# Optimization experiments

Measured on AMD Instinct MI355X. Metric: run time of the kernel, lower is better.

Reference implementation:

```python
import jax, jax.numpy as jnp
import numpy as np

N_NODES = 50000
N_EDGES = 1600000
IN_FEAT = 128
HEADS = 8
OUT_FEAT = 16


def setup_inputs() -> dict:
    key = jax.random.key(0)
    ks = jax.random.split(key, 8)
    feat = jax.random.normal(ks[0], (N_NODES, IN_FEAT), dtype=jnp.float32)
    src = jax.random.randint(ks[1], (N_EDGES,), 0, N_NODES, dtype=jnp.int32)
    dst = jax.random.randint(ks[2], (N_EDGES,), 0, N_NODES, dtype=jnp.int32)
    eps = jax.random.normal(ks[3], (N_EDGES, HEADS), dtype=jnp.float32)
    # small init scale keeps exp(log_scale) numerically tame
    W_fc = jax.random.normal(ks[4], (IN_FEAT, HEADS * OUT_FEAT), dtype=jnp.float32) * 0.05
    W_post = jax.random.normal(ks[5], (OUT_FEAT, 4), dtype=jnp.float32) * 0.05
    b_post = jax.random.normal(ks[6], (4,), dtype=jnp.float32) * 0.05
    bias = jax.random.normal(ks[7], (HEADS, OUT_FEAT), dtype=jnp.float32) * 0.05
    return {"feat": feat, "src": src, "dst": dst, "eps": eps,
            "W_fc": W_fc, "W_post": W_post, "b_post": b_post, "bias": bias}


def reference(feat, src, dst, eps, W_fc, W_post, b_post, bias):
    N = feat.shape[0]
    # node projection: [N, H, F]
    h = (feat @ W_fc).reshape(N, HEADS, OUT_FEAT)
    # per-node posterior params: [N, H, 4] -> loc_l, loc_r, log_scale_l, log_scale_r
    post = jnp.einsum('nhf,fk->nhk', h, W_post) + b_post
    loc_l, loc_r, lsl, lsr = post[..., 0], post[..., 1], post[..., 2], post[..., 3]
    # per-edge score via reparameterized sample: [E, H]
    loc = loc_l[src] + loc_r[dst]
    log_scale = lsl[src] + lsr[dst]
    e = loc + jnp.exp(log_scale) * eps
    # edge softmax over incoming edges of each dst node (per head)
    m = jax.lax.stop_gradient(jax.ops.segment_max(e, dst, num_segments=N))
    ex = jnp.exp(e - m[dst])
    denom = jax.ops.segment_sum(ex, dst, num_segments=N)
    a = ex / denom[dst]
    # weighted aggregation: sum over in-edges of h[src] * a
    msg = h[src] * a[:, :, None]                     # [E, H, F]
    out = jax.ops.segment_sum(msg, dst, num_segments=N)  # [N, H, F]
    out = out + bias[None]
    return out
```

## Files before the change

### kernel.cpp

```cpp
#include <hip/hip_runtime.h>
#include <hip/hip_fp16.h>

#define IN_FEAT 128
#define HEADS 8
#define OUT_FEAT 16
#define HF 128
#define BSHIFT 6
#define BNODES 64
#define NBMAX 1024
#define CHUNK 8192

__global__ __launch_bounds__(256) void gemm_post_kernel(
    const float* __restrict__ feat, const float* __restrict__ W_fc,
    const float* __restrict__ W_post, const float* __restrict__ b_post,
    __half* __restrict__ hbuf, float* __restrict__ post, int N)
{
    __shared__ float4 lds4[32 * 32];
    float* lds = (float*)lds4;
    const int tid = threadIdx.x;
    const int node_base = blockIdx.x * 32;

    const float4* f4 = (const float4*)feat;
    for (int i = tid; i < 32 * 32; i += 256) {
        int n = i >> 5, k4 = i & 31;
        int gn = node_base + n;
        float4 v = make_float4(0.f, 0.f, 0.f, 0.f);
        if (gn < N) v = f4[gn * 32 + k4];
        lds4[i] = v;
    }
    __syncthreads();

    const int cg = tid & 31, ng = tid >> 5;
    const int n0 = ng * 4;
    float acc[4][4];
#pragma unroll
    for (int i = 0; i < 4; i++) acc[i][0] = acc[i][1] = acc[i][2] = acc[i][3] = 0.f;

    const float4* W4 = (const float4*)W_fc;
#pragma unroll 4
    for (int k = 0; k < 128; ++k) {
        float4 w = W4[k * 32 + cg];
#pragma unroll
        for (int i = 0; i < 4; i++) {
            float f = lds[(n0 + i) * 128 + k];
            acc[i][0] += f * w.x; acc[i][1] += f * w.y;
            acc[i][2] += f * w.z; acc[i][3] += f * w.w;
        }
    }
    __half2* hb2 = (__half2*)hbuf;
#pragma unroll
    for (int i = 0; i < 4; i++) {
        int gn = node_base + n0 + i;
        if (gn < N) {
            union { uint2 u; __half2 h[2]; } pk;
            pk.h[0] = __floats2half2_rn(acc[i][0], acc[i][1]);
            pk.h[1] = __floats2half2_rn(acc[i][2], acc[i][3]);
            *(uint2*)&hb2[gn * 64 + cg * 2] = pk.u;
        }
    }
    __syncthreads();
#pragma unroll
    for (int i = 0; i < 4; i++)
        lds4[(n0 + i) * 32 + cg] = make_float4(acc[i][0], acc[i][1], acc[i][2], acc[i][3]);
    __syncthreads();

    {
        int n = tid >> 3, h = tid & 7;
        float p0 = b_post[0], p1 = b_post[1], p2 = b_post[2], p3 = b_post[3];
#pragma unroll
        for (int f = 0; f < 16; ++f) {
            float v = lds[n * 128 + h * 16 + f];
            p0 += v * W_post[f * 4 + 0];
            p1 += v * W_post[f * 4 + 1];
            p2 += v * W_post[f * 4 + 2];
            p3 += v * W_post[f * 4 + 3];
        }
        int gn = node_base + n;
        if (gn < N) {
            post[gn * 32 + 0 * 8 + h] = p0;
            post[gn * 32 + 1 * 8 + h] = p1;
            post[gn * 32 + 2 * 8 + h] = p2;
            post[gn * 32 + 3 * 8 + h] = p3;
        }
    }
}

__global__ __launch_bounds__(256) void bucket_hist_kernel(
    const int* __restrict__ dst, int* __restrict__ bucket_tot, int E, int nb)
{
    __shared__ int cnt[NBMAX];
    const int tid = threadIdx.x;
    for (int i = tid; i < nb; i += 256) cnt[i] = 0;
    __syncthreads();
    const int stride = gridDim.x * 256;
    for (int g = blockIdx.x * 256 + tid; g < E; g += stride)
        atomicAdd(&cnt[dst[g] >> BSHIFT], 1);
    __syncthreads();
    for (int i = tid; i < nb; i += 256) {
        int c = cnt[i];
        if (c) atomicAdd(&bucket_tot[i], c);
    }
}

__global__ __launch_bounds__(256) void bucket_scan_kernel(
    const int* __restrict__ bucket_tot, int* __restrict__ bucket_base,
    int* __restrict__ bucket_cursor, int nb, int E)
{
    __shared__ int sd[256];
    const int tid = threadIdx.x;
    int v[4]; int s = 0;
#pragma unroll
    for (int k = 0; k < 4; ++k) {
        int i = tid * 4 + k;
        v[k] = (i < nb) ? bucket_tot[i] : 0;
        s += v[k];
    }
    sd[tid] = s;
    __syncthreads();
    for (int off = 1; off < 256; off <<= 1) {
        int t = (tid >= off) ? sd[tid - off] : 0;
        __syncthreads();
        sd[tid] += t;
        __syncthreads();
    }
    int excl = sd[tid] - s;
#pragma unroll
    for (int k = 0; k < 4; ++k) {
        int i = tid * 4 + k;
        if (i < nb) { bucket_base[i] = excl; bucket_cursor[i] = excl; }
        excl += v[k];
    }
    if (tid == 0) bucket_base[nb] = E;
}

__global__ __launch_bounds__(256) void bucket_scatter_kernel(
    const int* __restrict__ src, const int* __restrict__ dst,
    int* __restrict__ bucket_cursor, uint2* __restrict__ recs, int E, int nb)
{
    __shared__ int cnt[NBMAX];
    __shared__ int base[NBMAX];
    const int tid = threadIdx.x;
    for (int i = tid; i < nb; i += 256) cnt[i] = 0;
    __syncthreads();
    const int e0 = blockIdx.x * CHUNK;
    const int e1 = min(e0 + CHUNK, E);
    for (int e = e0 + tid; e < e1; e += 256)
        atomicAdd(&cnt[dst[e] >> BSHIFT], 1);
    __syncthreads();
    for (int i = tid; i < nb; i += 256) {
        int c = cnt[i];
        base[i] = c ? atomicAdd(&bucket_cursor[i], c) : 0;
        cnt[i] = 0;
    }
    __syncthreads();
    for (int e = e0 + tid; e < e1; e += 256) {
        int d = dst[e];
        int b = d >> BSHIFT;
        int slot = base[b] + atomicAdd(&cnt[b], 1);
        recs[slot] = make_uint2((unsigned)e,
                                ((unsigned)src[e] << BSHIFT) | (unsigned)(d & (BNODES - 1)));
    }
}

__global__ __launch_bounds__(256) void bucket_csr_kernel(
    const uint2* __restrict__ recs, const int* __restrict__ bucket_base,
    int* __restrict__ offsets, uint2* __restrict__ csr, int N, int E)
{
    __shared__ int ncnt[BNODES];
    __shared__ int snc[BNODES];
    const int b = blockIdx.x, tid = threadIdx.x;
    const int node_lo = b << BSHIFT;
    const int rlo = bucket_base[b], rhi = bucket_base[b + 1];
    const int gn = node_lo + tid;

    if (tid < BNODES) ncnt[tid] = 0;
    __syncthreads();
    for (int r = rlo + tid; r < rhi; r += 256)
        atomicAdd(&ncnt[recs[r].y & (BNODES - 1u)], 1);
    __syncthreads();
    if (tid < BNODES) snc[tid] = ncnt[tid];
    __syncthreads();
    for (int off = 1; off < BNODES; off <<= 1) {
        int t = (tid < BNODES && tid >= off) ? snc[tid - off] : 0;
        __syncthreads();
        if (tid < BNODES) snc[tid] += t;
        __syncthreads();
    }
    int excl = (tid < BNODES) ? snc[tid] - ncnt[tid] : 0;
    if (tid < BNODES && gn < N) offsets[gn] = rlo + excl;
    if (b == 0 && tid == 0) offsets[N] = E;
    __syncthreads();
    if (tid < BNODES) ncnt[tid] = excl;
    __syncthreads();

    for (int r = rlo + tid; r < rhi; r += 256) {
        uint2 rec = recs[r];
        int dl = (int)(rec.y & (BNODES - 1u));
        unsigned s = rec.y >> BSHIFT;
        int slot = rlo + atomicAdd(&ncnt[dl], 1);
        csr[slot] = make_uint2(rec.x, s);
    }
}

__global__ __launch_bounds__(128) void agg_kernel(
    const uint2* __restrict__ csr, const int* __restrict__ offsets,
    const float* __restrict__ post, const float* __restrict__ eps,
    const __half* __restrict__ hbuf, const float* __restrict__ bias,
    float* __restrict__ out)
{
    __shared__ int    s_src[32];
    __shared__ float  s_a[32 * 9];
    __shared__ float  dpost[16];
    __shared__ float2 r_acc[64];
    __shared__ float  r_dsum[64];

    const int d = blockIdx.x;
    const int tid = threadIdx.x;
    const int wave = tid >> 6, lane = tid & 63;
    const int h = lane >> 3, fp = lane & 7;
    const int start = offsets[d];
    const int deg = offsets[d + 1] - start;

    if (tid < 16)
        dpost[tid] = post[d * 32 + ((tid < 8) ? (8 + tid) : (16 + tid))];
    __syncthreads();

    float2 acc = make_float2(0.f, 0.f);
    float dsum = 0.f;

    const float2* p2 = (const float2*)post;
    const float2* e2 = (const float2*)eps;

    for (int c = 0; c < deg; c += 32) {
        int jc = min(32, deg - c);
        if (tid < 4 * jc) {
            int j = tid >> 2, q = tid & 3;
            uint2 rec = csr[start + c + j];
            int e = (int)rec.x, s = (int)rec.y;
            if (q == 0) s_src[j] = s;
            float2 ll = p2[(size_t)s * 16 + q];
            float2 sl = p2[(size_t)s * 16 + 8 + q];
            float2 ep = e2[(size_t)e * 4 + q];
            int h0 = 2 * q;
            float ev0 = (ll.x + dpost[h0])     + __expf(sl.x + dpost[8 + h0])     * ep.x;
            float ev1 = (ll.y + dpost[h0 + 1]) + __expf(sl.y + dpost[8 + h0 + 1]) * ep.y;
            s_a[j * 9 + h0]     = __expf(ev0);
            s_a[j * 9 + h0 + 1] = __expf(ev1);
        }
        __syncthreads();
        for (int j = wave; j < jc; j += 2) {
            float a = s_a[j * 9 + h];
            const __half2* hr = (const __half2*)(hbuf + (size_t)s_src[j] * 128);
            float2 hv = __half22float2(hr[h * 8 + fp]);
            acc.x += a * hv.x;
            acc.y += a * hv.y;
            dsum  += a;
        }
        __syncthreads();
    }

    if (wave == 0) { r_acc[lane] = acc; r_dsum[lane] = dsum; }
    __syncthreads();
    if (wave == 1) {
        r_acc[lane].x += acc.x;
        r_acc[lane].y += acc.y;
        r_dsum[lane]  += dsum;
    }
    __syncthreads();
    if (wave == 0) {
        float2 A = r_acc[lane];
        float ds = r_dsum[lane];
        float inv = (ds > 0.f) ? 1.f / ds : 0.f;
        float2 o;
        o.x = A.x * inv + bias[h * 16 + 2 * fp];
        o.y = A.y * inv + bias[h * 16 + 2 * fp + 1];
        ((float2*)out)[(size_t)d * 64 + lane] = o;
    }
}

extern "C" void kernel_launch(void* const* d_in, const int* in_sizes, int n_in,
                              void* d_out, int out_size, void* d_ws, size_t ws_size,
                              hipStream_t stream)
{
    const float* feat   = (const float*)d_in[0];
    const int*   src    = (const int*)d_in[1];
    const int*   dst    = (const int*)d_in[2];
    const float* eps    = (const float*)d_in[3];
    const float* W_fc   = (const float*)d_in[4];
    const float* W_post = (const float*)d_in[5];
    const float* b_post = (const float*)d_in[6];
    const float* bias   = (const float*)d_in[7];
    float* out = (float*)d_out;

    const int N = in_sizes[0] / IN_FEAT;
    const int E = in_sizes[1];
    const int nb = (N + BNODES - 1) >> BSHIFT;

    char* p = (char*)d_ws;
    auto alloc = [&](size_t bytes) {
        char* r = p;
        p += (bytes + 255) & ~size_t(255);
        return r;
    };
    __half* hbuf    = (__half*)alloc((size_t)N * HF * 2);
    float*  post    = (float*)alloc((size_t)N * 32 * 4);
    int*    offsets = (int*)alloc((size_t)(N + 1) * 4);
    int*    bucket_tot    = (int*)alloc((size_t)(NBMAX + 1) * 4);
    int*    bucket_base   = (int*)alloc((size_t)(NBMAX + 1) * 4);
    int*    bucket_cursor = (int*)alloc((size_t)(NBMAX + 1) * 4);
    uint2*  recs    = (uint2*)alloc((size_t)E * 8);
    uint2*  csr     = (uint2*)alloc((size_t)E * 8);

    hipMemsetAsync(bucket_tot, 0, (size_t)(nb) * 4, stream);

    gemm_post_kernel<<<(N + 31) / 32, 256, 0, stream>>>(feat, W_fc, W_post, b_post,
                                                        hbuf, post, N);
    bucket_hist_kernel<<<512, 256, 0, stream>>>(dst, bucket_tot, E, nb);
    bucket_scan_kernel<<<1, 256, 0, stream>>>(bucket_tot, bucket_base,
                                              bucket_cursor, nb, E);
    bucket_scatter_kernel<<<(E + CHUNK - 1) / CHUNK, 256, 0, stream>>>(
        src, dst, bucket_cursor, recs, E, nb);
    bucket_csr_kernel<<<nb, 256, 0, stream>>>(recs, bucket_base, offsets, csr, N, E);
    agg_kernel<<<N, 128, 0, stream>>>(csr, offsets, post, eps, hbuf, bias, out);
}
```

Baseline: 360.8 us.

## Build CSR via per-node atomic counts and use one wave per destination node

Replaces the two-pass bucketed scatter (records, then per-bucket CSR) with a per-node histogram, a per-bucket wave scan, and a direct global-atomic scatter into CSR. This drops the intermediate record array and one full pass over the edges. The aggregation kernel is restructured so that one 64-lane wave handles each destination node. Edge scores are computed 8 edges at a time and broadcast with shuffles, which removes the LDS staging and the block-level syncs. The cost is heavy global atomic traffic on cursor[d], and edge order within each node becomes nondeterministic.

```diff
diff --git a/kernel.cpp b/kernel.cpp
--- a/kernel.cpp
+++ b/kernel.cpp
@@ -8,7 +8,6 @@
 #define BSHIFT 6
 #define BNODES 64
 #define NBMAX 1024
-#define CHUNK 8192
 
 __global__ __launch_bounds__(256) void gemm_post_kernel(
     const float* __restrict__ feat, const float* __restrict__ W_fc,
@@ -85,16 +84,20 @@
     }
 }
 
-__global__ __launch_bounds__(256) void bucket_hist_kernel(
-    const int* __restrict__ dst, int* __restrict__ bucket_tot, int E, int nb)
+__global__ __launch_bounds__(256) void hist_kernel(
+    const int* __restrict__ dst, int* __restrict__ ncnt,
+    int* __restrict__ bucket_tot, int E, int nb)
 {
     __shared__ int cnt[NBMAX];
     const int tid = threadIdx.x;
     for (int i = tid; i < nb; i += 256) cnt[i] = 0;
     __syncthreads();
     const int stride = gridDim.x * 256;
-    for (int g = blockIdx.x * 256 + tid; g < E; g += stride)
-        atomicAdd(&cnt[dst[g] >> BSHIFT], 1);
+    for (int g = blockIdx.x * 256 + tid; g < E; g += stride) {
+        int d = dst[g];
+        atomicAdd(&ncnt[d], 1);
+        atomicAdd(&cnt[d >> BSHIFT], 1);
+    }
     __syncthreads();
     for (int i = tid; i < nb; i += 256) {
         int c = cnt[i];
@@ -104,7 +107,7 @@
 
 __global__ __launch_bounds__(256) void bucket_scan_kernel(
     const int* __restrict__ bucket_tot, int* __restrict__ bucket_base,
-    int* __restrict__ bucket_cursor, int nb, int E)
+    int nb, int E)
 {
     __shared__ int sd[256];
     const int tid = threadIdx.x;
@@ -127,155 +130,103 @@
 #pragma unroll
     for (int k = 0; k < 4; ++k) {
         int i = tid * 4 + k;
-        if (i < nb) { bucket_base[i] = excl; bucket_cursor[i] = excl; }
+        if (i < nb) bucket_base[i] = excl;
         excl += v[k];
     }
     if (tid == 0) bucket_base[nb] = E;
 }
 
-__global__ __launch_bounds__(256) void bucket_scatter_kernel(
+__global__ __launch_bounds__(256) void node_scan_kernel(
+    const int* __restrict__ ncnt, const int* __restrict__ bucket_base,
+    int* __restrict__ offsets, int* __restrict__ cursor, int N, int nb, int E)
+{
+    if (blockIdx.x == 0 && threadIdx.x == 0) offsets[N] = E;
+    const int b = blockIdx.x * 4 + (threadIdx.x >> 6);
+    const int lane = threadIdx.x & 63;
+    if (b >= nb) return;
+    const int node = (b << BSHIFT) + lane;
+    int v = (node < N) ? ncnt[node] : 0;
+    int s = v;
+#pragma unroll
+    for (int off = 1; off < 64; off <<= 1) {
+        int t = __shfl_up(s, off, 64);
+        if (lane >= off) s += t;
+    }
+    int excl = bucket_base[b] + s - v;
+    if (node < N) { offsets[node] = excl; cursor[node] = excl; }
+}
+
+__global__ __launch_bounds__(256) void scatter_kernel(
     const int* __restrict__ src, const int* __restrict__ dst,
-    int* __restrict__ bucket_cursor, uint2* __restrict__ recs, int E, int nb)
-{
-    __shared__ int cnt[NBMAX];
-    __shared__ int base[NBMAX];
-    const int tid = threadIdx.x;
-    for (int i = tid; i < nb; i += 256) cnt[i] = 0;
-    __syncthreads();
-    const int e0 = blockIdx.x * CHUNK;
-    const int e1 = min(e0 + CHUNK, E);
-    for (int e = e0 + tid; e < e1; e += 256)
-        atomicAdd(&cnt[dst[e] >> BSHIFT], 1);
-    __syncthreads();
-    for (int i = tid; i < nb; i += 256) {
-        int c = cnt[i];
-        base[i] = c ? atomicAdd(&bucket_cursor[i], c) : 0;
-        cnt[i] = 0;
-    }
-    __syncthreads();
-    for (int e = e0 + tid; e < e1; e += 256) {
+    int* __restrict__ cursor, uint2* __restrict__ csr, int E)
+{
+    const int stride = gridDim.x * 256;
+    for (int e = blockIdx.x * 256 + threadIdx.x; e < E; e += stride) {
         int d = dst[e];
-        int b = d >> BSHIFT;
-        int slot = base[b] + atomicAdd(&cnt[b], 1);
-        recs[slot] = make_uint2((unsigned)e,
-                                ((unsigned)src[e] << BSHIFT) | (unsigned)(d & (BNODES - 1)));
-    }
-}
-
-__global__ __launch_bounds__(256) void bucket_csr_kernel(
-    const uint2* __restrict__ recs, const int* __restrict__ bucket_base,
-    int* __restrict__ offsets, uint2* __restrict__ csr, int N, int E)
-{
-    __shared__ int ncnt[BNODES];
-    __shared__ int snc[BNODES];
-    const int b = blockIdx.x, tid = threadIdx.x;
-    const int node_lo = b << BSHIFT;
-    const int rlo = bucket_base[b], rhi = bucket_base[b + 1];
-    const int gn = node_lo + tid;
-
-    if (tid < BNODES) ncnt[tid] = 0;
-    __syncthreads();
-    for (int r = rlo + tid; r < rhi; r += 256)
-        atomicAdd(&ncnt[recs[r].y & (BNODES - 1u)], 1);
-    __syncthreads();
-    if (tid < BNODES) snc[tid] = ncnt[tid];
-    __syncthreads();
-    for (int off = 1; off < BNODES; off <<= 1) {
-        int t = (tid < BNODES && tid >= off) ? snc[tid - off] : 0;
-        __syncthreads();
-        if (tid < BNODES) snc[tid] += t;
-        __syncthreads();
-    }
-    int excl = (tid < BNODES) ? snc[tid] - ncnt[tid] : 0;
-    if (tid < BNODES && gn < N) offsets[gn] = rlo + excl;
-    if (b == 0 && tid == 0) offsets[N] = E;
-    __syncthreads();
-    if (tid < BNODES) ncnt[tid] = excl;
-    __syncthreads();
-
-    for (int r = rlo + tid; r < rhi; r += 256) {
-        uint2 rec = recs[r];
-        int dl = (int)(rec.y & (BNODES - 1u));
-        unsigned s = rec.y >> BSHIFT;
-        int slot = rlo + atomicAdd(&ncnt[dl], 1);
-        csr[slot] = make_uint2(rec.x, s);
-    }
-}
-
-__global__ __launch_bounds__(128) void agg_kernel(
+        int slot = atomicAdd(&cursor[d], 1);
+        csr[slot] = make_uint2((unsigned)e, (unsigned)src[e]);
+    }
+}
+
+__global__ __launch_bounds__(256) void agg_kernel(
     const uint2* __restrict__ csr, const int* __restrict__ offsets,
     const float* __restrict__ post, const float* __restrict__ eps,
     const __half* __restrict__ hbuf, const float* __restrict__ bias,
-    float* __restrict__ out)
-{
-    __shared__ int    s_src[32];
-    __shared__ float  s_a[32 * 9];
-    __shared__ float  dpost[16];
-    __shared__ float2 r_acc[64];
-    __shared__ float  r_dsum[64];
-
-    const int d = blockIdx.x;
-    const int tid = threadIdx.x;
-    const int wave = tid >> 6, lane = tid & 63;
-    const int h = lane >> 3, fp = lane & 7;
+    float* __restrict__ out, int N)
+{
+    const int lane = threadIdx.x & 63;
+    const int d = blockIdx.x * 4 + (threadIdx.x >> 6);
+    if (d >= N) return;
     const int start = offsets[d];
     const int deg = offsets[d + 1] - start;
-
-    if (tid < 16)
-        dpost[tid] = post[d * 32 + ((tid < 8) ? (8 + tid) : (16 + tid))];
-    __syncthreads();
+    const int j = lane >> 3, hh = lane & 7;
+    const int h = j;
+    const float dl  = post[d * 32 + 8 + hh];
+    const float dls = post[d * 32 + 24 + hh];
 
     float2 acc = make_float2(0.f, 0.f);
     float dsum = 0.f;
 
-    const float2* p2 = (const float2*)post;
-    const float2* e2 = (const float2*)eps;
-
-    for (int c = 0; c < deg; c += 32) {
-        int jc = min(32, deg - c);
-        if (tid < 4 * jc) {
-            int j = tid >> 2, q = tid & 3;
-            uint2 rec = csr[start + c + j];
-            int e = (int)rec.x, s = (int)rec.y;
-            if (q == 0) s_src[j] = s;
-            float2 ll = p2[(size_t)s * 16 + q];
-            float2 sl = p2[(size_t)s * 16 + 8 + q];
-            float2 ep = e2[(size_t)e * 4 + q];
-            int h0 = 2 * q;
-            float ev0 = (ll.x + dpost[h0])     + __expf(sl.x + dpost[8 + h0])     * ep.x;
-            float ev1 = (ll.y + dpost[h0 + 1]) + __expf(sl.y + dpost[8 + h0 + 1]) * ep.y;
-            s_a[j * 9 + h0]     = __expf(ev0);
-            s_a[j * 9 + h0 + 1] = __expf(ev1);
-        }
-        __syncthreads();
-        for (int j = wave; j < jc; j += 2) {
-            float a = s_a[j * 9 + h];
-            const __half2* hr = (const __half2*)(hbuf + (size_t)s_src[j] * 128);
-            float2 hv = __half22float2(hr[h * 8 + fp]);
+    int c = 0;
+    for (; c + 8 <= deg; c += 8) {
+        uint2 rec = csr[start + c + j];
+        int e = (int)rec.x, s = (int)rec.y;
+        float ll = post[s * 32 + hh];
+        float sl = post[s * 32 + 16 + hh];
+        float ep = eps[(size_t)e * 8 + hh];
+        float ex = __expf((ll + dl) + __expf(sl + dls) * ep);
+#pragma unroll
+        for (int jj = 0; jj < 8; ++jj) {
+            float a = __shfl(ex, jj * 8 + h, 64);
+            int  sj = __shfl(s, jj * 8, 64);
+            float2 hv = __half22float2(((const __half2*)(hbuf + (size_t)sj * HF))[lane]);
             acc.x += a * hv.x;
             acc.y += a * hv.y;
-            dsum  += a;
-        }
-        __syncthreads();
-    }
-
-    if (wave == 0) { r_acc[lane] = acc; r_dsum[lane] = dsum; }
-    __syncthreads();
-    if (wave == 1) {
-        r_acc[lane].x += acc.x;
-        r_acc[lane].y += acc.y;
-        r_dsum[lane]  += dsum;
-    }
-    __syncthreads();
-    if (wave == 0) {
-        float2 A = r_acc[lane];
-        float ds = r_dsum[lane];
-        float inv = (ds > 0.f) ? 1.f / ds : 0.f;
-        float2 o;
-        o.x = A.x * inv + bias[h * 16 + 2 * fp];
-        o.y = A.y * inv + bias[h * 16 + 2 * fp + 1];
-        ((float2*)out)[(size_t)d * 64 + lane] = o;
-    }
+            dsum += a;
+        }
+    }
+    if (c < deg) {
+        int jc = deg - c;
+        uint2 rec = csr[start + c + min(j, jc - 1)];
+        int e = (int)rec.x, s = (int)rec.y;
+        float ll = post[s * 32 + hh];
+        float sl = post[s * 32 + 16 + hh];
+        float ep = eps[(size_t)e * 8 + hh];
+        float ex = (j < jc) ? __expf((ll + dl) + __expf(sl + dls) * ep) : 0.f;
+        for (int jj = 0; jj < jc; ++jj) {
+            float a = __shfl(ex, jj * 8 + h, 64);
+            int  sj = __shfl(s, jj * 8, 64);
+            float2 hv = __half22float2(((const __half2*)(hbuf + (size_t)sj * HF))[lane]);
+            acc.x += a * hv.x;
+            acc.y += a * hv.y;
+            dsum += a;
+        }
+    }
+
+    float inv = (dsum > 0.f) ? 1.f / dsum : 0.f;
+    float2 bv = ((const float2*)bias)[lane];
+    float2 o = make_float2(acc.x * inv + bv.x, acc.y * inv + bv.y);
+    ((float2*)out)[(size_t)d * 64 + lane] = o;
 }
 
 extern "C" void kernel_launch(void* const* d_in, const int* in_sizes, int n_in,
@@ -305,21 +256,22 @@
     __half* hbuf    = (__half*)alloc((size_t)N * HF * 2);
     float*  post    = (float*)alloc((size_t)N * 32 * 4);
     int*    offsets = (int*)alloc((size_t)(N + 1) * 4);
-    int*    bucket_tot    = (int*)alloc((size_t)(NBMAX + 1) * 4);
-    int*    bucket_base   = (int*)alloc((size_t)(NBMAX + 1) * 4);
-    int*    bucket_cursor = (int*)alloc((size_t)(NBMAX + 1) * 4);
-    uint2*  recs    = (uint2*)alloc((size_t)E * 8);
+    int*    ncnt    = (int*)alloc((size_t)N * 4);
+    int*    cursor  = (int*)alloc((size_t)N * 4);
+    int*    bucket_tot  = (int*)alloc((size_t)(NBMAX + 1) * 4);
+    int*    bucket_base = (int*)alloc((size_t)(NBMAX + 1) * 4);
     uint2*  csr     = (uint2*)alloc((size_t)E * 8);
 
-    hipMemsetAsync(bucket_tot, 0, (size_t)(nb) * 4, stream);
+    hipMemsetAsync(bucket_tot, 0, (size_t)nb * 4, stream);
+    hipMemsetAsync(ncnt, 0, (size_t)N * 4, stream);
 
     gemm_post_kernel<<<(N + 31) / 32, 256, 0, stream>>>(feat, W_fc, W_post, b_post,
                                                         hbuf, post, N);
-    bucket_hist_kernel<<<512, 256, 0, stream>>>(dst, bucket_tot, E, nb);
-    bucket_scan_kernel<<<1, 256, 0, stream>>>(bucket_tot, bucket_base,
-                                              bucket_cursor, nb, E);
-    bucket_scatter_kernel<<<(E + CHUNK - 1) / CHUNK, 256, 0, stream>>>(
-        src, dst, bucket_cursor, recs, E, nb);
-    bucket_csr_kernel<<<nb, 256, 0, stream>>>(recs, bucket_base, offsets, csr, N, E);
-    agg_kernel<<<N, 128, 0, stream>>>(csr, offsets, post, eps, hbuf, bias, out);
-}
+    hist_kernel<<<512, 256, 0, stream>>>(dst, ncnt, bucket_tot, E, nb);
+    bucket_scan_kernel<<<1, 256, 0, stream>>>(bucket_tot, bucket_base, nb, E);
+    node_scan_kernel<<<(nb + 3) / 4, 256, 0, stream>>>(ncnt, bucket_base,
+                                                       offsets, cursor, N, nb, E);
+    scatter_kernel<<<2048, 256, 0, stream>>>(src, dst, cursor, csr, E);
+    agg_kernel<<<(N + 3) / 4, 256, 0, stream>>>(csr, offsets, post, eps, hbuf,
+                                                bias, out, N);
+}
```

After: 450.8 us. 1.25x slower.

## Aggregate each destination node with one wave using shuffles instead of LDS

Applied to the files above, without the earlier changes.

Rewrites the aggregation kernel so each 64-lane wave handles one destination node, with four nodes per 256-thread block. Edge scores are computed 8 edges at a time with 8 lanes per edge, then broadcast via wave shuffles, removing shared memory, block barriers and the two-wave reduction. This trades intra-node parallelism across two waves for barrier-free execution and more independent nodes in flight.

```diff
diff --git a/kernel.cpp b/kernel.cpp
--- a/kernel.cpp
+++ b/kernel.cpp
@@ -202,80 +202,65 @@
     }
 }
 
-__global__ __launch_bounds__(128) void agg_kernel(
+__global__ __launch_bounds__(256) void agg_kernel(
     const uint2* __restrict__ csr, const int* __restrict__ offsets,
     const float* __restrict__ post, const float* __restrict__ eps,
     const __half* __restrict__ hbuf, const float* __restrict__ bias,
-    float* __restrict__ out)
-{
-    __shared__ int    s_src[32];
-    __shared__ float  s_a[32 * 9];
-    __shared__ float  dpost[16];
-    __shared__ float2 r_acc[64];
-    __shared__ float  r_dsum[64];
-
-    const int d = blockIdx.x;
-    const int tid = threadIdx.x;
-    const int wave = tid >> 6, lane = tid & 63;
-    const int h = lane >> 3, fp = lane & 7;
+    float* __restrict__ out, int N)
+{
+    const int lane = threadIdx.x & 63;
+    const int d = blockIdx.x * 4 + (threadIdx.x >> 6);
+    if (d >= N) return;
     const int start = offsets[d];
     const int deg = offsets[d + 1] - start;
-
-    if (tid < 16)
-        dpost[tid] = post[d * 32 + ((tid < 8) ? (8 + tid) : (16 + tid))];
-    __syncthreads();
+    const int j = lane >> 3, hh = lane & 7;
+    const int h = j;
+    const float dl  = post[d * 32 + 8 + hh];
+    const float dls = post[d * 32 + 24 + hh];
 
     float2 acc = make_float2(0.f, 0.f);
     float dsum = 0.f;
 
-    const float2* p2 = (const float2*)post;
-    const float2* e2 = (const float2*)eps;
-
-    for (int c = 0; c < deg; c += 32) {
-        int jc = min(32, deg - c);
-        if (tid < 4 * jc) {
-            int j = tid >> 2, q = tid & 3;
-            uint2 rec = csr[start + c + j];
-            int e = (int)rec.x, s = (int)rec.y;
-            if (q == 0) s_src[j] = s;
-            float2 ll = p2[(size_t)s * 16 + q];
-            float2 sl = p2[(size_t)s * 16 + 8 + q];
-            float2 ep = e2[(size_t)e * 4 + q];
-            int h0 = 2 * q;
-            float ev0 = (ll.x + dpost[h0])     + __expf(sl.x + dpost[8 + h0])     * ep.x;
-            float ev1 = (ll.y + dpost[h0 + 1]) + __expf(sl.y + dpost[8 + h0 + 1]) * ep.y;
-            s_a[j * 9 + h0]     = __expf(ev0);
-            s_a[j * 9 + h0 + 1] = __expf(ev1);
-        }
-        __syncthreads();
-        for (int j = wave; j < jc; j += 2) {
-            float a = s_a[j * 9 + h];
-            const __half2* hr = (const __half2*)(hbuf + (size_t)s_src[j] * 128);
-            float2 hv = __half22float2(hr[h * 8 + fp]);
+    int c = 0;
+    for (; c + 8 <= deg; c += 8) {
+        uint2 rec = csr[start + c + j];
+        int e = (int)rec.x, s = (int)rec.y;
+        float ll = post[s * 32 + hh];
+        float sl = post[s * 32 + 16 + hh];
+        float ep = eps[(size_t)e * 8 + hh];
+        float ex = __expf((ll + dl) + __expf(sl + dls) * ep);
+#pragma unroll
+        for (int jj = 0; jj < 8; ++jj) {
+            float a = __shfl(ex, jj * 8 + h, 64);
+            int  sj = __shfl(s, jj * 8, 64);
+            float2 hv = __half22float2(((const __half2*)(hbuf + (size_t)sj * HF))[lane]);
             acc.x += a * hv.x;
             acc.y += a * hv.y;
-            dsum  += a;
-        }
-        __syncthreads();
-    }
-
-    if (wave == 0) { r_acc[lane] = acc; r_dsum[lane] = dsum; }
-    __syncthreads();
-    if (wave == 1) {
-        r_acc[lane].x += acc.x;
-        r_acc[lane].y += acc.y;
-        r_dsum[lane]  += dsum;
-    }
-    __syncthreads();
-    if (wave == 0) {
-        float2 A = r_acc[lane];
-        float ds = r_dsum[lane];
-        float inv = (ds > 0.f) ? 1.f / ds : 0.f;
-        float2 o;
-        o.x = A.x * inv + bias[h * 16 + 2 * fp];
-        o.y = A.y * inv + bias[h * 16 + 2 * fp + 1];
-        ((float2*)out)[(size_t)d * 64 + lane] = o;
-    }
+            dsum += a;
+        }
+    }
+    if (c < deg) {
+        int jc = deg - c;
+        uint2 rec = csr[start + c + min(j, jc - 1)];
+        int e = (int)rec.x, s = (int)rec.y;
+        float ll = post[s * 32 + hh];
+        float sl = post[s * 32 + 16 + hh];
+        float ep = eps[(size_t)e * 8 + hh];
+        float ex = (j < jc) ? __expf((ll + dl) + __expf(sl + dls) * ep) : 0.f;
+        for (int jj = 0; jj < jc; ++jj) {
+            float a = __shfl(ex, jj * 8 + h, 64);
+            int  sj = __shfl(s, jj * 8, 64);
+            float2 hv = __half22float2(((const __half2*)(hbuf + (size_t)sj * HF))[lane]);
+            acc.x += a * hv.x;
+            acc.y += a * hv.y;
+            dsum += a;
+        }
+    }
+
+    float inv = (dsum > 0.f) ? 1.f / dsum : 0.f;
+    float2 bv = ((const float2*)bias)[lane];
+    float2 o = make_float2(acc.x * inv + bv.x, acc.y * inv + bv.y);
+    ((float2*)out)[(size_t)d * 64 + lane] = o;
 }
 
 extern "C" void kernel_launch(void* const* d_in, const int* in_sizes, int n_in,
@@ -311,7 +296,7 @@
     uint2*  recs    = (uint2*)alloc((size_t)E * 8);
     uint2*  csr     = (uint2*)alloc((size_t)E * 8);
 
-    hipMemsetAsync(bucket_tot, 0, (size_t)(nb) * 4, stream);
+    hipMemsetAsync(bucket_tot, 0, (size_t)nb * 4, stream);
 
     gemm_post_kernel<<<(N + 31) / 32, 256, 0, stream>>>(feat, W_fc, W_post, b_post,
                                                         hbuf, post, N);
@@ -321,5 +306,6 @@
     bucket_scatter_kernel<<<(E + CHUNK - 1) / CHUNK, 256, 0, stream>>>(
         src, dst, bucket_cursor, recs, E, nb);
     bucket_csr_kernel<<<nb, 256, 0, stream>>>(recs, bucket_base, offsets, csr, N, E);
-    agg_kernel<<<N, 128, 0, stream>>>(csr, offsets, post, eps, hbuf, bias, out);
-}
+    agg_kernel<<<(N + 3) / 4, 256, 0, stream>>>(csr, offsets, post, eps, hbuf,
+                                                bias, out, N);
+}
```

After: 333.4 us. 7.6% less time.
